# Kernel optimization log

Measured on AMD Instinct MI355X. Metric: run time of the kernel, lower is better.

The kernel has to match this reference:

```python
import jax, jax.numpy as jnp
import numpy as np

N, H, DK, DV, DFF, D = 2, 8, 32, 32, 512, 256
B, S = 2, 2048
MASK_VALUE = -1e-30
EPS = 1e-14  # K.epsilon()**2 with default epsilon 1e-7


def glorot(key, shape):
    fan_in, fan_out = shape[-2], shape[-1]
    limit = np.sqrt(6.0 / (fan_in + fan_out))
    return jax.random.uniform(key, shape, jnp.float32, -limit, limit)


def setup_inputs() -> dict:
    key = jax.random.key(0)
    ks = jax.random.split(key, 8)
    return {
        "x": jax.random.normal(ks[0], (B, S, D), jnp.float32),
        "mask": jnp.ones((B, S), jnp.float32),
        "Wq": glorot(ks[1], (N, H, D, DK)),
        "Wk": glorot(ks[2], (N, H, D, DK)),
        "Wv": glorot(ks[3], (N, H, D, DV)),
        "Wo": glorot(ks[4], (N, H * DV, D)),
        "W1": glorot(ks[5], (N, D, DFF)),
        "b1": jnp.zeros((N, DFF), jnp.float32),
        "W2": glorot(ks[6], (N, DFF, D)),
        "b2": jnp.zeros((N, D), jnp.float32),
        "gamma": jnp.ones((2 * N,), jnp.float32),
        "beta": jnp.zeros((2 * N,), jnp.float32),
    }


def _layernorm(x, g, b):
    mean = jnp.mean(x, axis=-1, keepdims=True)
    var = jnp.mean(jnp.square(x - mean), axis=-1, keepdims=True)
    return (x - mean) / jnp.sqrt(var + EPS) * g + b


def reference(x, mask, Wq, Wk, Wv, Wo, W1, b1, W2, b2, gamma, beta):
    m = mask[:, None, None, :]  # [B,1,1,S], multiplies score rows' key axis
    for i in range(N):
        # batched multi-head attention (no 1/sqrt(dk) scaling, faithful to source)
        q = jnp.einsum("bsd,hdk->bhsk", x, Wq[i])
        k = jnp.einsum("bsd,hdk->bhsk", x, Wk[i])
        v = jnp.einsum("bsd,hdv->bhsv", x, Wv[i])
        A = jnp.einsum("bhsk,bhtk->bhst", q, k)  # [B,H,S,S]
        A = m * A + (1.0 - m) * MASK_VALUE
        A = jax.nn.softmax(A, axis=-1)
        o = jnp.einsum("bhst,bhtv->bhsv", A, v)
        conc = o.transpose(0, 2, 1, 3).reshape(x.shape[0], x.shape[1], H * DV)
        x = x + conc @ Wo[i]
        x = _layernorm(x, gamma[2 * i], beta[2 * i])
        ffn = jax.nn.relu(x @ W1[i] + b1[i]) @ W2[i] + b2[i]
        x = x + ffn
        x = _layernorm(x, gamma[2 * i + 1], beta[2 * i + 1])
    return x
```

## Files before the change

### kernel.cpp

```cpp
#include <hip/hip_runtime.h>
#include <hip/hip_bf16.h>

#define NL 2
#define NH 8
#define DKk 32
#define DVv 32
#define DFF 512
#define DD 256
#define BB 2
#define SS 2048
#define MROWS (BB*SS)
#define LN_EPS 1e-14f
#define L2E 1.4426950408889634f
#define SOFT_SHIFT_L2E (50.0f*L2E)

typedef __hip_bfloat16 bf16;
typedef unsigned short us;
typedef short bf16x8 __attribute__((ext_vector_type(8)));
typedef float f32x4  __attribute__((ext_vector_type(4)));
typedef unsigned short us4 __attribute__((ext_vector_type(4)));

#define O_XF   256
#define O_QB   (O_XF+1048576)
#define O_KH   (O_QB+1048576)
#define O_KL   (O_KH+524288)
#define O_VT   (O_KL+524288)
#define O_XH   (O_VT+524288)
#define O_XL   (O_XH+524288)
#define O_OP   (O_XL+524288)
#define O_ML   (O_OP+2097152)
#define O_MASK (O_ML+65536)
#define O_B1   (O_MASK+4096)
#define O_B2   (O_B1+1024)
#define O_GM   (O_B2+512)
#define O_BT   (O_GM+4)
#define O_PREP (O_BT+4)
#define CONV_TOTAL (1048576+4096+1024+512+4+4)
#define CONV_BLOCKS ((CONV_TOTAL+255)/256)
#define PREP_BLOCKS 512
#define PQH 0u
#define PQL 393216u
#define POH 786432u
#define POL 917504u
#define P1H 1048576u
#define P1L 1310720u
#define P2H 1572864u
#define P2L 1835008u

__device__ __forceinline__ float us2f(us u){
  unsigned int v = ((unsigned int)u) << 16; float f;
  __builtin_memcpy(&f, &v, 4); return f;
}
__device__ __forceinline__ us f2bf_rne(float f){
  unsigned int b = __float_as_uint(f);
  b += 0x7FFFu + ((b>>16)&1u);
  return (us)(b>>16);
}

#if __has_builtin(__builtin_amdgcn_exp2f)
#define EXP2F(x) __builtin_amdgcn_exp2f(x)
#else
#define EXP2F(x) exp2f(x)
#endif

#if __has_builtin(__builtin_amdgcn_cvt_pk_bf16_f32)
typedef __bf16 bf16x2_t __attribute__((ext_vector_type(2)));
__device__ __forceinline__ int pack_bf16(float a, float b){
  bf16x2_t r = __builtin_amdgcn_cvt_pk_bf16_f32(a, b);
  int i; __builtin_memcpy(&i, &r, 4); return i;
}
#else
__device__ __forceinline__ int pack_bf16(float a, float b){
  int b0 = __float_as_int(a) + 0x8000;
  int b1 = __float_as_int(b) + 0x8000;
  return (b1 & 0xFFFF0000) | ((int)((unsigned)b0 >> 16));
}
#endif

__device__ __forceinline__ void gl_lds16(const us* g, us* l){
  __builtin_amdgcn_global_load_lds(
    (const __attribute__((address_space(1))) unsigned int*)g,
    (__attribute__((address_space(3))) unsigned int*)l, 16, 0, 0);
}

__device__ __forceinline__ size_t xhl_idx(int row, int col){
  int rt = row>>6, rg = (row>>4)&3, L15 = row&15;
  int kc = col>>5, Q = (col>>3)&3, j = col&7;
  return ((size_t)(rt*8+kc))*2048 + rg*512 + Q*128 + L15*8 + j;
}

__device__ __forceinline__ float conv1(const void* src, size_t i, int flag){
  if(flag) return ((const float*)src)[i];
  return us2f(((const us*)src)[i]);
}

__device__ __forceinline__ void prep_b_raw(const void* W0, const void* W1v, const void* W2v,
                                           int baseoff, us* __restrict__ Bh, us* __restrict__ Bl,
                                           int Kd, int Nd, int qkv, int g, int flag)
{
  int total = (Kd/32)*(Nd/16)*64;
  if(g >= total) return;
  int lane = g & 63, fi = g >> 6;
  int ncN = Nd/16;
  int nc = fi % ncN, kc = fi / ncN;
  int Q = lane>>4, L15 = lane&15;
  int n = nc*16 + L15;
  const void* src;
  int off0, stride;
  if(qkv){
    int sec = n>>8, h = (n>>5)&7, kq = n&31;
    src = (sec==0)?W0:((sec==1)?W1v:W2v);
    off0 = baseoff + h*8192 + kq;
    stride = 32;
  } else {
    src = W0;
    off0 = baseoff + n;
    stride = Nd;
  }
  #pragma unroll
  for(int j=0;j<8;j++){
    int k = kc*32 + Q*8 + j;
    float v = conv1(src, (size_t)off0 + (size_t)k*stride, flag);
    us hb = f2bf_rne(v);
    Bh[(size_t)g*8 + j] = hb;
    Bl[(size_t)g*8 + j] = f2bf_rne(v - us2f(hb));
  }
}

__global__ void conv_prep(const void* s0, const void* s1, const void* sWq, const void* sWk,
                          const void* sWv, const void* sWo, const void* sW1, const void* sb1,
                          const void* sW2, const void* sb2, const void* sgm, const void* sbt,
                          float* __restrict__ ws, int* __restrict__ flagp)
{
  __shared__ int fsh[4];
  int bad = 0;
  const us* xr = (const us*)s0;
  for(int i=threadIdx.x; i<4096; i+=256){
    float f = us2f(xr[i]);
    if(!(fabsf(f) < 1e3f)) bad = 1;
  }
  unsigned long long m = __ballot(bad);
  if((threadIdx.x&63)==0) fsh[threadIdx.x>>6] = (m!=0ull);
  __syncthreads();
  int flag = (fsh[0]|fsh[1]|fsh[2]|fsh[3]);
  if(blockIdx.x==0 && threadIdx.x==0) *flagp = flag;

  int b = blockIdx.x;
  if(b < PREP_BLOCKS){
    int layer = b >> 8, lb = b & 255;
    us* prep = (us*)(ws + O_PREP);
    if(lb < 96){
      int g = lb*256 + threadIdx.x;
      prep_b_raw(sWq, sWk, sWv, layer*65536, prep+PQH+(size_t)layer*196608,
                 prep+PQL+(size_t)layer*196608, 256, 768, 1, g, flag);
    } else if(lb < 128){
      int g = (lb-96)*256 + threadIdx.x;
      prep_b_raw(sWo, nullptr, nullptr, layer*65536, prep+POH+(size_t)layer*65536,
                 prep+POL+(size_t)layer*65536, 256, 256, 0, g, flag);
    } else if(lb < 192){
      int g = (lb-128)*256 + threadIdx.x;
      prep_b_raw(sW1, nullptr, nullptr, layer*131072, prep+P1H+(size_t)layer*131072,
                 prep+P1L+(size_t)layer*131072, 256, 512, 0, g, flag);
    } else {
      int g = (lb-192)*256 + threadIdx.x;
      prep_b_raw(sW2, nullptr, nullptr, layer*131072, prep+P2H+(size_t)layer*131072,
                 prep+P2L+(size_t)layer*131072, 512, 256, 0, g, flag);
    }
    return;
  }
  int g = (b - PREP_BLOCKS)*256 + threadIdx.x;
  if(g < 1048576){
    float v = conv1(s0, g, flag);
    ws[O_XF+g] = v;
    us hb = f2bf_rne(v);
    us lb = f2bf_rne(v - us2f(hb));
    size_t xi = xhl_idx(g>>8, g&255);
    ((us*)(ws+O_XH))[xi] = hb;
    ((us*)(ws+O_XL))[xi] = lb;
    return;
  }
  g -= 1048576;
  if(g < 4096){ ws[O_MASK+g] = conv1(s1, g, flag)*L2E; return; }
  g -= 4096;
  if(g < 1024){ ws[O_B1+g] = conv1(sb1, g, flag); return; }
  g -= 1024;
  if(g < 512){ ws[O_B2+g] = conv1(sb2, g, flag); return; }
  g -= 512;
  if(g < 4){ ws[O_GM+g] = conv1(sgm, g, flag); return; }
  g -= 4;
  if(g < 4){ ws[O_BT+g] = conv1(sbt, g, flag); return; }
}

template<int MODE>
__launch_bounds__(256)
__global__ void gemm_mfma(const us* __restrict__ Axh, const us* __restrict__ Axl,
                          const us* __restrict__ Bh, const us* __restrict__ Bl,
                          const float* __restrict__ bias,
                          float* __restrict__ O,
                          us* __restrict__ QH, us* __restrict__ QL,
                          us* __restrict__ KH, us* __restrict__ KL, us* __restrict__ VT,
                          int Ncols, int Kdim)
{
  __shared__ __align__(16) us SH[9216];
  us* Ah = SH; us* Al = SH+2048; us* Bhs = SH+4096; us* Bls = SH+6144;
  const int t = threadIdx.x;
  const int w = t>>6, lane = t&63;
  const int Q = lane>>4, L15 = lane&15;
  const int row0 = blockIdx.x*64;
  const int nc0 = blockIdx.y*4;
  const int col0 = blockIdx.y*64;

  f32x4 acc[2][2];
  #pragma unroll
  for(int i=0;i<2;i++)
    #pragma unroll
    for(int j=0;j<2;j++) acc[i][j] = (f32x4){0.f,0.f,0.f,0.f};

  const int nKc = Kdim>>5;
  const int ncW = Ncols>>4;

  for(int kc=0; kc<nKc; kc++){
    {
      size_t abase = ((size_t)(blockIdx.x*nKc + kc))*2048;
      gl_lds16(&Axh[abase + (size_t)t*8], &Ah[t*8]);
      gl_lds16(&Axl[abase + (size_t)t*8], &Al[t*8]);
      size_t gidx = ((size_t)(kc*ncW + nc0 + w)*64 + lane)*8;
      gl_lds16(&Bh[gidx], &Bhs[t*8]);
      gl_lds16(&Bl[gidx], &Bls[t*8]);
    }
    __syncthreads();

    bf16x8 aAh[2], aAl[2], bBh[2], bBl[2];
    #pragma unroll
    for(int rg2=0;rg2<2;rg2++){
      int rg = (w&1)*2 + rg2;
      aAh[rg2] = *(const bf16x8*)&Ah[rg*512 + lane*8];
      aAl[rg2] = *(const bf16x8*)&Al[rg*512 + lane*8];
    }
    #pragma unroll
    for(int cg2=0;cg2<2;cg2++){
      int nc = (w>>1)*2 + cg2;
      bBh[cg2] = *(const bf16x8*)&Bhs[nc*512 + lane*8];
      bBl[cg2] = *(const bf16x8*)&Bls[nc*512 + lane*8];
    }
    #pragma unroll
    for(int rg2=0;rg2<2;rg2++)
      #pragma unroll
      for(int cg2=0;cg2<2;cg2++){
        acc[rg2][cg2] = __builtin_amdgcn_mfma_f32_16x16x32_bf16(aAl[rg2], bBh[cg2], acc[rg2][cg2], 0,0,0);
        acc[rg2][cg2] = __builtin_amdgcn_mfma_f32_16x16x32_bf16(aAh[rg2], bBl[cg2], acc[rg2][cg2], 0,0,0);
        acc[rg2][cg2] = __builtin_amdgcn_mfma_f32_16x16x32_bf16(aAh[rg2], bBh[cg2], acc[rg2][cg2], 0,0,0);
      }
    __syncthreads();
  }

  if(MODE==0){
    us* TH = SH;
    us* TL = SH + 4608;
    #pragma unroll
    for(int rg2=0;rg2<2;rg2++)
      #pragma unroll
      for(int cg2=0;cg2<2;cg2++)
        #pragma unroll
        for(int r=0;r<4;r++){
          int rl = (w&1)*32 + rg2*16 + Q*4 + r;
          int cl = (w>>1)*32 + cg2*16 + L15;
          float va = acc[rg2][cg2][r];
          us hb = f2bf_rne(va);
          TH[rl*72+cl] = hb;
          TL[rl*72+cl] = f2bf_rne(va - us2f(hb));
        }
    __syncthreads();
    const int sec = col0>>8;
    const int h0  = (col0&255)>>5;
    const int b_  = row0>>11;
    const int srow0 = row0 & 2047;
    if(sec < 2){
      us* DH = (sec==0) ? QH : KH;
      us* DL = (sec==0) ? QL : KL;
      #pragma unroll
      for(int u2=0; u2<2; u2++){
        int u = w + u2*4;
        int rg = u&3, half = u>>2;
        int lbase = (rg*16 + L15)*72 + half*32 + Q*8;
        bf16x8 hv = *(const bf16x8*)&TH[lbase];
        bf16x8 lv = *(const bf16x8*)&TL[lbase];
        int bh = b_*NH + h0 + half;
        size_t dbase = ((size_t)(bh*128 + (srow0>>4) + rg)*64 + lane)*8;
        *(bf16x8*)&DH[dbase] = hv;
        *(bf16x8*)&DL[dbase] = lv;
      }
    } else {
      #pragma unroll
      for(int u2=0; u2<2; u2++){
        int u = w + u2*4;
        int sgrp = u&1, kqh = (u>>1)&1, half = u>>2;
        union{ us u8[8]; bf16x8 v; } vv;
        #pragma unroll
        for(int j=0;j<8;j++){
          int rl = sgrp*32 + Q*8 + j;
          int cl = half*32 + kqh*16 + L15;
          vv.u8[j] = TH[rl*72+cl];
        }
        int bh = b_*NH + h0 + half;
        size_t dbase = ((size_t)((bh*64 + (srow0>>5) + sgrp)*2 + kqh)*64 + lane)*8;
        *(bf16x8*)&VT[dbase] = vv.v;
      }
    }
  } else {
    #pragma unroll
    for(int rg2=0;rg2<2;rg2++)
      #pragma unroll
      for(int cg2=0;cg2<2;cg2++)
        #pragma unroll
        for(int r=0;r<4;r++){
          int row = row0 + (w&1)*32 + rg2*16 + Q*4 + r;
          int c   = col0 + (w>>1)*32 + cg2*16 + L15;
          float v = acc[rg2][cg2][r] + bias[c];
          O[(size_t)row*Ncols + c] = v>0.f ? v : 0.f;
        }
  }
}

template<int SRC>
__launch_bounds__(256)
__global__ void gemm_ln(const float* __restrict__ A,
                        const float* __restrict__ OpartA, const float* __restrict__ MLA,
                        const us* __restrict__ Bh, const us* __restrict__ Bl,
                        const float* __restrict__ bias, const float* __restrict__ res,
                        float* __restrict__ xf,
                        us* __restrict__ xh, us* __restrict__ xl,
                        const float* __restrict__ gamma, const float* __restrict__ beta, int gi,
                        void* __restrict__ out, int write_out,
                        const int* __restrict__ flagp, int Kdim)
{
  __shared__ __align__(16) us Ah[512], Al[512];
  __shared__ __align__(16) us Bhs[8192], Bls[8192];
  __shared__ float lred[128];
  const int t = threadIdx.x;
  const int w = t>>6, lane = t&63;
  const int Q = lane>>4, L15 = lane&15;
  const int row0 = blockIdx.x*16;
  const int nKc = Kdim>>5;

  f32x4 acc[4];
  #pragma unroll
  for(int cg=0;cg<4;cg++) acc[cg] = (f32x4){0.f,0.f,0.f,0.f};

  for(int kc=0; kc<nKc; kc++){
    if(t < 128){
      int r = t>>3;
      int kl = (t&7)*4;
      float4 v;
      if(SRC==0){
        int row = row0 + r;
        int b_ = row>>11, s_ = row&2047;
        size_t i0 = (size_t)(b_*8 + kc)*2048 + s_;
        float l = MLA[i0] + MLA[i0+32768];
        float inv = 1.f/l;
        float4 o0 = *(const float4*)&OpartA[i0*32 + kl];
        float4 o1 = *(const float4*)&OpartA[(i0+32768)*32 + kl];
        v.x=(o0.x+o1.x)*inv; v.y=(o0.y+o1.y)*inv;
        v.z=(o0.z+o1.z)*inv; v.w=(o0.w+o1.w)*inv;
      } else {
        v = *(const float4*)&A[(size_t)(row0+r)*Kdim + kc*32 + kl];
      }
      float f[4] = {v.x, v.y, v.z, v.w};
      us4 h4, l4;
      #pragma unroll
      for(int j=0;j<4;j++){
        us hb = f2bf_rne(f[j]);
        h4[j] = hb; l4[j] = f2bf_rne(f[j] - us2f(hb));
      }
      int off = (kl>>3)*128 + r*8 + (kl&7);
      *(us4*)&Ah[off] = h4;
      *(us4*)&Al[off] = l4;
    }
    #pragma unroll
    for(int ii=0; ii<4; ii++){
      int unit = w + ii*4;
      size_t gidx = ((size_t)(kc*16 + unit)*64 + lane)*8;
      gl_lds16(&Bh[gidx], &Bhs[unit*512 + lane*8]);
      gl_lds16(&Bl[gidx], &Bls[unit*512 + lane*8]);
    }
    __syncthreads();

    bf16x8 aAh = *(const bf16x8*)&Ah[lane*8];
    bf16x8 aAl = *(const bf16x8*)&Al[lane*8];
    #pragma unroll
    for(int cg=0;cg<4;cg++){
      int unit = w*4 + cg;
      bf16x8 bBh = *(const bf16x8*)&Bhs[unit*512 + lane*8];
      bf16x8 bBl = *(const bf16x8*)&Bls[unit*512 + lane*8];
      acc[cg] = __builtin_amdgcn_mfma_f32_16x16x32_bf16(aAl, bBh, acc[cg], 0,0,0);
      acc[cg] = __builtin_amdgcn_mfma_f32_16x16x32_bf16(aAh, bBl, acc[cg], 0,0,0);
      acc[cg] = __builtin_amdgcn_mfma_f32_16x16x32_bf16(aAh, bBh, acc[cg], 0,0,0);
    }
    __syncthreads();
  }

  float tmp[4][4];
  #pragma unroll
  for(int cg=0;cg<4;cg++)
    #pragma unroll
    for(int r=0;r<4;r++){
      int row = row0 + Q*4 + r;
      int c = w*64 + cg*16 + L15;
      float v = acc[cg][r] + res[(size_t)row*DD + c];
      if(SRC==1) v += bias[c];
      tmp[cg][r] = v;
    }
  float s[4], sq[4];
  #pragma unroll
  for(int r=0;r<4;r++){
    s[r]  = tmp[0][r]+tmp[1][r]+tmp[2][r]+tmp[3][r];
    sq[r] = tmp[0][r]*tmp[0][r]+tmp[1][r]*tmp[1][r]+tmp[2][r]*tmp[2][r]+tmp[3][r]*tmp[3][r];
  }
  #pragma unroll
  for(int off=1; off<16; off<<=1)
    #pragma unroll
    for(int r=0;r<4;r++){
      s[r]  += __shfl_xor(s[r], off);
      sq[r] += __shfl_xor(sq[r], off);
    }
  if(L15==0){
    #pragma unroll
    for(int r=0;r<4;r++){
      int rl = Q*4 + r;
      lred[(w*16 + rl)*2]   = s[r];
      lred[(w*16 + rl)*2+1] = sq[r];
    }
  }
  __syncthreads();
  float g = gamma[gi], bb = beta[gi];
  float scv[4], mnv[4];
  #pragma unroll
  for(int r=0;r<4;r++){
    int rl = Q*4 + r;
    float S  = lred[rl*2]   + lred[(16+rl)*2]   + lred[(32+rl)*2]   + lred[(48+rl)*2];
    float SQ = lred[rl*2+1] + lred[(16+rl)*2+1] + lred[(32+rl)*2+1] + lred[(48+rl)*2+1];
    float mean = S*(1.f/DD);
    float var  = SQ*(1.f/DD) - mean*mean;
    scv[r] = rsqrtf(var+LN_EPS)*g;
    mnv[r] = mean;
  }
  int flag = write_out ? *flagp : 0;
  #pragma unroll
  for(int cg=0;cg<4;cg++)
    #pragma unroll
    for(int r=0;r<4;r++){
      int row = row0 + Q*4 + r;
      int c = w*64 + cg*16 + L15;
      float val = (tmp[cg][r]-mnv[r])*scv[r] + bb;
      xf[(size_t)row*DD + c] = val;
      us hb = f2bf_rne(val);
      size_t xi = xhl_idx(row, c);
      xh[xi] = hb;
      xl[xi] = f2bf_rne(val - us2f(hb));
      if(write_out){
        if(flag) ((float*)out)[(size_t)row*DD + c] = val;
        else     ((bf16*)out)[(size_t)row*DD + c] = __float2bfloat16(val);
      }
    }
}

__launch_bounds__(256)
__global__ void attn_kernel(const us* __restrict__ QH, const us* __restrict__ QL,
                            const us* __restrict__ KH, const us* __restrict__ KL,
                            const us* __restrict__ VT,
                            const float* __restrict__ mask,
                            float* __restrict__ Opart, float* __restrict__ ML)
{
  __shared__ __align__(16) us Khs[4096], Kls[4096], Vts[4096];
  __shared__ __align__(16) float Msl[128];
  const int t = threadIdx.x;
  const int bh = blockIdx.x >> 6;
  const int qt = (blockIdx.x & 63) >> 1;
  const int ks = blockIdx.x & 1;
  const int b_ = bh >> 3;
  const int wv = t >> 6;
  const int lane = t & 63;
  const int Q = lane >> 4, L15 = lane & 15;
  const int q0 = qt*64 + wv*16;

  size_t qidx = ((size_t)(bh*128 + qt*4 + wv)*64 + lane)*8;
  const bf16x8 qh_v = *(const bf16x8*)&QH[qidx];
  const bf16x8 ql_v = *(const bf16x8*)&QL[qidx];

  const us* KHbh = KH + (size_t)bh*65536;
  const us* KLbh = KL + (size_t)bh*65536;
  const us* VTbh = VT + (size_t)bh*65536;

  f32x4 Oa0a = {0.f,0.f,0.f,0.f}, Oa0b = {0.f,0.f,0.f,0.f};
  f32x4 Oa1a = {0.f,0.f,0.f,0.f}, Oa1b = {0.f,0.f,0.f,0.f};
  float lacc = 0.f;

  const int kend = ks*1024 + 1024;
  for(int t0 = ks*1024; t0 < kend; t0 += 128){
    {
      size_t kbase = (size_t)(t0>>4)*512;
      size_t vbase = (size_t)(t0>>5)*1024;
      #pragma unroll
      for(int ii=0; ii<2; ii++){
        int s = t + ii*256;
        gl_lds16(&KHbh[kbase + (size_t)s*8], &Khs[s*8]);
        gl_lds16(&KLbh[kbase + (size_t)s*8], &Kls[s*8]);
        gl_lds16(&VTbh[vbase + (size_t)s*8], &Vts[s*8]);
      }
      if(t < 128) Msl[t] = mask[b_*SS + t0 + t];
    }
    __syncthreads();

    f32x4 St[8];
    const f32x4 zz = {0.f,0.f,0.f,0.f};
    #pragma unroll
    for(int kt=0;kt<8;kt++){
      bf16x8 aKh = *(const bf16x8*)&Khs[kt*512 + lane*8];
      bf16x8 aKl = *(const bf16x8*)&Kls[kt*512 + lane*8];
      f32x4 a = __builtin_amdgcn_mfma_f32_16x16x32_bf16(aKl, qh_v, zz, 0,0,0);
      a = __builtin_amdgcn_mfma_f32_16x16x32_bf16(aKh, ql_v, a, 0,0,0);
      a = __builtin_amdgcn_mfma_f32_16x16x32_bf16(aKh, qh_v, a, 0,0,0);
      St[kt] = a;
    }

    float lsum = 0.f;
    #pragma unroll
    for(int kt=0;kt<8;kt++){
      float4 mv = *(const float4*)&Msl[kt*16 + Q*4];
      float mvr[4] = {mv.x, mv.y, mv.z, mv.w};
      #pragma unroll
      for(int r=0;r<4;r++){
        float p = EXP2F(fmaf(mvr[r], St[kt][r], -SOFT_SHIFT_L2E));
        St[kt][r] = p;
        lsum += p;
      }
    }
    lacc += lsum;

    int pk[8][2];
    #pragma unroll
    for(int kt=0;kt<8;kt++){
      pk[kt][0] = pack_bf16(St[kt][0], St[kt][1]);
      pk[kt][1] = pack_bf16(St[kt][2], St[kt][3]);
    }

    #pragma unroll
    for(int c=0;c<4;c++){
      union { int i[4]; bf16x8 v; } bu;
      #pragma unroll
      for(int d=0;d<4;d++){
        int srcl = (((Q&1)*2 + (d>>1))<<4) | L15;
        int vlo = __shfl(pk[2*c  ][d&1], srcl, 64);
        int vhi = __shfl(pk[2*c+1][d&1], srcl, 64);
        bu.i[d] = (Q & 2) ? vhi : vlo;
      }
      bf16x8 aV0 = *(const bf16x8*)&Vts[(c*2+0)*512 + lane*8];
      bf16x8 aV1 = *(const bf16x8*)&Vts[(c*2+1)*512 + lane*8];
      if(c < 2){
        Oa0a = __builtin_amdgcn_mfma_f32_16x16x32_bf16(aV0, bu.v, Oa0a, 0,0,0);
        Oa1a = __builtin_amdgcn_mfma_f32_16x16x32_bf16(aV1, bu.v, Oa1a, 0,0,0);
      } else {
        Oa0b = __builtin_amdgcn_mfma_f32_16x16x32_bf16(aV0, bu.v, Oa0b, 0,0,0);
        Oa1b = __builtin_amdgcn_mfma_f32_16x16x32_bf16(aV1, bu.v, Oa1b, 0,0,0);
      }
    }
    __syncthreads();
  }

  f32x4 Oa0 = Oa0a + Oa0b;
  f32x4 Oa1 = Oa1a + Oa1b;
  lacc += __shfl_xor(lacc, 16);
  lacc += __shfl_xor(lacc, 32);

  float* opp = &Opart[((size_t)(ks*16+bh)*SS + q0 + L15)*32];
  #pragma unroll
  for(int r=0;r<4;r++){
    opp[Q*4+r]    = Oa0[r];
    opp[16+Q*4+r] = Oa1[r];
  }
  if(Q==0){
    ML[(size_t)(ks*16+bh)*SS + q0 + L15] = lacc;
  }
}

extern "C" void kernel_launch(void* const* d_in, const int* in_sizes, int n_in,
                              void* d_out, int out_size, void* d_ws, size_t ws_size,
                              hipStream_t stream)
{
  float* ws = (float*)d_ws;
  int* flagp = (int*)d_ws;

  float* xf  = ws + O_XF;
  us* QHb = (us*)(ws + O_QB);
  us* QLb = QHb + 1048576;
  us* KH = (us*)(ws + O_KH);
  us* KL = (us*)(ws + O_KL);
  us* VT = (us*)(ws + O_VT);
  us* XH = (us*)(ws + O_XH);
  us* XL = (us*)(ws + O_XL);
  float* Opart = ws + O_OP;
  float* ML  = ws + O_ML;
  float* fh  = Opart;
  float* b1f = ws + O_B1;
  float* b2f_ = ws + O_B2;
  float* gmf = ws + O_GM;
  float* btf = ws + O_BT;
  us* prep = (us*)(ws + O_PREP);

  conv_prep<<<PREP_BLOCKS+CONV_BLOCKS,256,0,stream>>>(
      d_in[0], d_in[1], d_in[2], d_in[3], d_in[4], d_in[5],
      d_in[6], d_in[7], d_in[8], d_in[9], d_in[10], d_in[11],
      ws, flagp);

  for(int i=0;i<NL;i++){
    const float* b1i = b1f + (size_t)i*DFF;
    const float* b2i = b2f_ + (size_t)i*DD;

    dim3 g0(64, 12);
    gemm_mfma<0><<<g0,256,0,stream>>>(XH, XL,
                                      prep+PQH+(size_t)i*196608, prep+PQL+(size_t)i*196608,
                                      nullptr, nullptr,
                                      QHb, QLb, KH, KL, VT, 768, 256);
    attn_kernel<<<1024,256,0,stream>>>(QHb, QLb, KH, KL, VT, ws + O_MASK, Opart, ML);
    gemm_ln<0><<<256,256,0,stream>>>(nullptr, Opart, ML,
                                     prep+POH+(size_t)i*65536, prep+POL+(size_t)i*65536,
                                     nullptr, xf, xf, XH, XL,
                                     gmf, btf, 2*i, d_out, 0, flagp, 256);
    dim3 g2(64, 8);
    gemm_mfma<2><<<g2,256,0,stream>>>(XH, XL,
                                      prep+P1H+(size_t)i*131072, prep+P1L+(size_t)i*131072,
                                      b1i, fh,
                                      nullptr, nullptr, nullptr, nullptr, nullptr, 512, 256);
    gemm_ln<1><<<256,256,0,stream>>>(fh, nullptr, nullptr,
                                     prep+P2H+(size_t)i*131072, prep+P2L+(size_t)i*131072,
                                     b2i, xf, xf, XH, XL,
                                     gmf, btf, 2*i+1, d_out, (i==NL-1)?1:0, flagp, 512);
  }
}
```

Measured before the change: 270.7 us.

## Double-buffer K/V tiles in attention with smaller 64-key steps

The attention loop now stages K-high, K-low, V-transposed and mask tiles into two alternating LDS buffers of 64 keys each. Each iteration issues the async global-to-LDS loads for the next tile before computing on the current one, so memory latency can overlap the MFMA and exp work. This also drops the trailing barrier, leaving one barrier per iteration instead of two. The cost is twice as many iterations and barriers over the same key range, and the tile ordering has to stay correct across the two buffers.

```diff
diff --git a/kernel.cpp b/kernel.cpp
--- a/kernel.cpp
+++ b/kernel.cpp
@@ -490,33 +490,42 @@
   const us* KHbh = KH + (size_t)bh*65536;
   const us* KLbh = KL + (size_t)bh*65536;
   const us* VTbh = VT + (size_t)bh*65536;
+  const int base = ks*1024;
 
   f32x4 Oa0a = {0.f,0.f,0.f,0.f}, Oa0b = {0.f,0.f,0.f,0.f};
   f32x4 Oa1a = {0.f,0.f,0.f,0.f}, Oa1b = {0.f,0.f,0.f,0.f};
   float lacc = 0.f;
 
-  const int kend = ks*1024 + 1024;
-  for(int t0 = ks*1024; t0 < kend; t0 += 128){
-    {
-      size_t kbase = (size_t)(t0>>4)*512;
-      size_t vbase = (size_t)(t0>>5)*1024;
-      #pragma unroll
-      for(int ii=0; ii<2; ii++){
-        int s = t + ii*256;
-        gl_lds16(&KHbh[kbase + (size_t)s*8], &Khs[s*8]);
-        gl_lds16(&KLbh[kbase + (size_t)s*8], &Kls[s*8]);
-        gl_lds16(&VTbh[vbase + (size_t)s*8], &Vts[s*8]);
-      }
-      if(t < 128) Msl[t] = mask[b_*SS + t0 + t];
-    }
+  {
+    size_t kbase = (size_t)(base>>4)*512;
+    size_t vbase = (size_t)(base>>5)*1024;
+    gl_lds16(&KHbh[kbase + (size_t)t*8], &Khs[t*8]);
+    gl_lds16(&KLbh[kbase + (size_t)t*8], &Kls[t*8]);
+    gl_lds16(&VTbh[vbase + (size_t)t*8], &Vts[t*8]);
+    if(t < 64) Msl[t] = mask[b_*SS + base + t];
+  }
+
+  for(int s=0; s<16; s++){
     __syncthreads();
-
-    f32x4 St[8];
+    if(s < 15){
+      int t0n = base + (s+1)*64;
+      int bn = (s+1)&1;
+      size_t kbase = (size_t)(t0n>>4)*512;
+      size_t vbase = (size_t)(t0n>>5)*1024;
+      gl_lds16(&KHbh[kbase + (size_t)t*8], &Khs[bn*2048 + t*8]);
+      gl_lds16(&KLbh[kbase + (size_t)t*8], &Kls[bn*2048 + t*8]);
+      gl_lds16(&VTbh[vbase + (size_t)t*8], &Vts[bn*2048 + t*8]);
+      if(t < 64) Msl[bn*64 + t] = mask[b_*SS + t0n + t];
+    }
+    const int bo = (s&1)*2048;
+    const int mo = (s&1)*64;
+
+    f32x4 St[4];
     const f32x4 zz = {0.f,0.f,0.f,0.f};
     #pragma unroll
-    for(int kt=0;kt<8;kt++){
-      bf16x8 aKh = *(const bf16x8*)&Khs[kt*512 + lane*8];
-      bf16x8 aKl = *(const bf16x8*)&Kls[kt*512 + lane*8];
+    for(int kt=0;kt<4;kt++){
+      bf16x8 aKh = *(const bf16x8*)&Khs[bo + kt*512 + lane*8];
+      bf16x8 aKl = *(const bf16x8*)&Kls[bo + kt*512 + lane*8];
       f32x4 a = __builtin_amdgcn_mfma_f32_16x16x32_bf16(aKl, qh_v, zz, 0,0,0);
       a = __builtin_amdgcn_mfma_f32_16x16x32_bf16(aKh, ql_v, a, 0,0,0);
       a = __builtin_amdgcn_mfma_f32_16x16x32_bf16(aKh, qh_v, a, 0,0,0);
@@ -525,8 +534,8 @@
 
     float lsum = 0.f;
     #pragma unroll
-    for(int kt=0;kt<8;kt++){
-      float4 mv = *(const float4*)&Msl[kt*16 + Q*4];
+    for(int kt=0;kt<4;kt++){
+      float4 mv = *(const float4*)&Msl[mo + kt*16 + Q*4];
       float mvr[4] = {mv.x, mv.y, mv.z, mv.w};
       #pragma unroll
       for(int r=0;r<4;r++){
@@ -537,15 +546,15 @@
     }
     lacc += lsum;
 
-    int pk[8][2];
-    #pragma unroll
-    for(int kt=0;kt<8;kt++){
+    int pk[4][2];
+    #pragma unroll
+    for(int kt=0;kt<4;kt++){
       pk[kt][0] = pack_bf16(St[kt][0], St[kt][1]);
       pk[kt][1] = pack_bf16(St[kt][2], St[kt][3]);
     }
 
     #pragma unroll
-    for(int c=0;c<4;c++){
+    for(int c=0;c<2;c++){
       union { int i[4]; bf16x8 v; } bu;
       #pragma unroll
       for(int d=0;d<4;d++){
@@ -554,9 +563,9 @@
         int vhi = __shfl(pk[2*c+1][d&1], srcl, 64);
         bu.i[d] = (Q & 2) ? vhi : vlo;
       }
-      bf16x8 aV0 = *(const bf16x8*)&Vts[(c*2+0)*512 + lane*8];
-      bf16x8 aV1 = *(const bf16x8*)&Vts[(c*2+1)*512 + lane*8];
-      if(c < 2){
+      bf16x8 aV0 = *(const bf16x8*)&Vts[bo + (c*2+0)*512 + lane*8];
+      bf16x8 aV1 = *(const bf16x8*)&Vts[bo + (c*2+1)*512 + lane*8];
+      if(c == 0){
         Oa0a = __builtin_amdgcn_mfma_f32_16x16x32_bf16(aV0, bu.v, Oa0a, 0,0,0);
         Oa1a = __builtin_amdgcn_mfma_f32_16x16x32_bf16(aV1, bu.v, Oa1a, 0,0,0);
       } else {
@@ -564,7 +573,6 @@
         Oa1b = __builtin_amdgcn_mfma_f32_16x16x32_bf16(aV1, bu.v, Oa1b, 0,0,0);
       }
     }
-    __syncthreads();
   }
 
   f32x4 Oa0 = Oa0a + Oa0b;
```

Result: no change. 269.2 us (-0.5%).
